# Performance work log

Measured on AMD Instinct MI355X. Metric: run time of the kernel, lower is better.

## Reference

```python
import jax, jax.numpy as jnp
import numpy as np
from jax import lax

IN_PLANES = 512
GROWTH = 32
PLANES = 4 * GROWTH  # 128
EPS = 1e-5


def setup_inputs() -> dict:
    key = jax.random.key(0)
    ks = jax.random.split(key, 10)
    x = jax.random.normal(ks[0], (128, IN_PLANES, 32, 32), dtype=jnp.float32)
    # bn1 affine params (batch-stat BN, track_running_stats=False)
    gamma1 = jax.random.normal(ks[1], (IN_PLANES,), dtype=jnp.float32) * 0.1 + 1.0
    beta1 = jax.random.normal(ks[2], (IN_PLANES,), dtype=jnp.float32) * 0.1
    # convbn1: 1x1 conv weight + folded BN (running stats)
    w1 = jax.random.normal(ks[3], (PLANES, IN_PLANES, 1, 1), dtype=jnp.float32) * (1.0 / np.sqrt(IN_PLANES))
    gamma2 = jax.random.normal(ks[4], (PLANES,), dtype=jnp.float32) * 0.1 + 1.0
    beta2 = jax.random.normal(ks[5], (PLANES,), dtype=jnp.float32) * 0.1
    mean2 = jax.random.normal(ks[6], (PLANES,), dtype=jnp.float32) * 0.1
    var2 = jax.random.uniform(ks[7], (PLANES,), dtype=jnp.float32, minval=0.5, maxval=1.5)
    # conv2: 3x3 conv, padding 1, no bias
    w2 = jax.random.normal(ks[8], (GROWTH, PLANES, 3, 3), dtype=jnp.float32) * (1.0 / np.sqrt(9 * PLANES))
    return {"x": x, "gamma1": gamma1, "beta1": beta1, "w1": w1,
            "gamma2": gamma2, "beta2": beta2, "mean2": mean2, "var2": var2,
            "w2": w2}


def _bn(h, mean, var, gamma, beta):
    # channel-wise affine normalization, NCHW
    inv = lax.rsqrt(var + EPS)
    scale = (gamma * inv)[None, :, None, None]
    shift = (beta - mean * gamma * inv)[None, :, None, None]
    return h * scale + shift


def reference(x, gamma1, beta1, w1, gamma2, beta2, mean2, var2, w2):
    # bn1: batch statistics (track_running_stats=False)
    mu = jnp.mean(x, axis=(0, 2, 3))
    var = jnp.var(x, axis=(0, 2, 3))  # biased, as torch BN normalization
    h = _bn(x, mu, var, gamma1, beta1)
    h = jax.nn.relu(h)
    # convbn1: 1x1 conv then folded BN (running stats)
    h = lax.conv_general_dilated(h, w1, (1, 1), 'VALID',
                                 dimension_numbers=('NCHW', 'OIHW', 'NCHW'))
    h = _bn(h, mean2, var2, gamma2, beta2)
    h = jax.nn.relu(h)
    # conv2: 3x3, stride 1, pad 1, no bias
    out = lax.conv_general_dilated(h, w2, (1, 1), ((1, 1), (1, 1)),
                                   dimension_numbers=('NCHW', 'OIHW', 'NCHW'))
    # dense concat along channels
    return jnp.concatenate([x, out], axis=1)
```

## Files before the change

### kernel.cpp

```cpp
#include <hip/hip_runtime.h>

#define EPS 1e-5f

typedef __bf16 bf16x8 __attribute__((ext_vector_type(8)));
typedef __bf16 bf16x4 __attribute__((ext_vector_type(4)));
typedef unsigned short ushort8 __attribute__((ext_vector_type(8)));
typedef float f32x4 __attribute__((ext_vector_type(4)));

static __device__ __forceinline__ unsigned short f2bf(float f) {
  unsigned int u = __float_as_uint(f);
  u += 0x7fffu + ((u >> 16) & 1u);
  return (unsigned short)(u >> 16);
}


__global__ void __launch_bounds__(256) k1_kernel(
    const float* __restrict__ x, float* __restrict__ out,
    float* __restrict__ psum, float* __restrict__ psq,
    const float* __restrict__ w1, const float* __restrict__ gamma2,
    const float* __restrict__ beta2, const float* __restrict__ mean2,
    const float* __restrict__ var2, const float* __restrict__ w2,
    unsigned short* __restrict__ w1b, unsigned short* __restrict__ w2b,
    float* __restrict__ bias2) {
  const int t = threadIdx.x;
  if (blockIdx.x >= 4096) {
    int idx = (blockIdx.x - 4096) * 256 + t;
    if (idx < 128 * 512) {
      int oc = idx >> 9;
      float s2 = gamma2[oc] * rsqrtf(var2[oc] + EPS);
      w1b[idx] = f2bf(w1[idx] * s2);
    } else if (idx < 128 * 512 + 32 * 1152) {
      int i2 = idx - 128 * 512;
      int oc = i2 / 1152;
      int rem = i2 - oc * 1152;
      int tap = rem >> 7;
      int c = rem & 127;
      w2b[i2] = f2bf(w2[(oc * 128 + c) * 9 + tap]);
    } else if (idx < 128 * 512 + 32 * 1152 + 128) {
      int oc = idx - (128 * 512 + 32 * 1152);
      float s2 = gamma2[oc] * rsqrtf(var2[oc] + EPS);
      bias2[oc] = beta2[oc] - mean2[oc] * s2;
    }
    return;
  }
  const int c = blockIdx.x & 511;
  const int nq = blockIdx.x >> 9;
  float sum = 0.f, sq = 0.f;
  const f32x4* __restrict__ x4 = (const f32x4*)x;
  f32x4* out4 = (f32x4*)out;
#pragma unroll 8
  for (int i = 0; i < 16; ++i) {
    const int n = nq * 16 + i;
    f32x4 v = x4[(((size_t)n * 512 + c) << 8) + t];
    __builtin_nontemporal_store(v, &out4[(((size_t)n * 544 + c) << 8) + t]);
    sum += v[0] + v[1] + v[2] + v[3];
    sq += v[0] * v[0] + v[1] * v[1] + v[2] * v[2] + v[3] * v[3];
  }
  __shared__ float ls[2][4];
  for (int off = 32; off > 0; off >>= 1) {
    sum += __shfl_down(sum, off);
    sq += __shfl_down(sq, off);
  }
  const int w = t >> 6;
  if ((t & 63) == 0) { ls[0][w] = sum; ls[1][w] = sq; }
  __syncthreads();
  if (t == 0) {
    psum[c * 8 + nq] = ls[0][0] + ls[0][1] + ls[0][2] + ls[0][3];
    psq[c * 8 + nq] = ls[1][0] + ls[1][1] + ls[1][2] + ls[1][3];
  }
}

__global__ void reduce_kernel(const float* __restrict__ psum,
                              const float* __restrict__ psq,
                              const float* __restrict__ g1,
                              const float* __restrict__ be1,
                              float* __restrict__ s1, float* __restrict__ b1) {
  int c = blockIdx.x * 256 + threadIdx.x;
  if (c < 512) {
    float S = 0.f, Q = 0.f;
#pragma unroll
    for (int q = 0; q < 8; ++q) { S += psum[c * 8 + q]; Q += psq[c * 8 + q]; }
    float mean = S * (1.0f / 131072.0f);
    float var = Q * (1.0f / 131072.0f) - mean * mean;
    float s = g1[c] * rsqrtf(var + EPS);
    s1[c] = s;
    b1[c] = be1[c] - mean * s;
  }
}

__global__ void __launch_bounds__(256, 2) conv1_kernel(
    const float* __restrict__ x, const unsigned short* __restrict__ w1b,
    const float* __restrict__ s1, const float* __restrict__ b1,
    const float* __restrict__ bias2, unsigned short* __restrict__ h2) {
  const int t = threadIdx.x;
  __shared__ float s1s[512], b1s[512];
  __shared__ __align__(16) unsigned short tile[32 * 260];
  for (int cc = t; cc < 512; cc += 256) {
    s1s[cc] = s1[cc];
    b1s[cc] = b1[cc];
  }
  __syncthreads();

  const int lane = t & 63;
  const int wv = t >> 6;
  const int n = 127 - (blockIdx.x >> 2);
  const int q = blockIdx.x & 3;
  const int l15 = lane & 15;
  const int kb = lane >> 4;

  f32x4 acc[8][4];
#pragma unroll
  for (int m = 0; m < 8; ++m)
#pragma unroll
    for (int g = 0; g < 4; ++g) acc[m][g] = (f32x4){0.f, 0.f, 0.f, 0.f};

  const f32x4* __restrict__ xq = (const f32x4*)(x + (size_t)n * 524288 + q * 256);

  f32x4 v[8];
#pragma unroll
  for (int i = 0; i < 8; ++i)
    v[i] = xq[(size_t)(wv * 8 + i) * 256 + lane];

  for (int k = 0; k < 16; ++k) {
    const int c0 = k * 32;
#pragma unroll
    for (int i = 0; i < 8; ++i) {
      const int c = c0 + wv * 8 + i;
      const float s = s1s[c], b = b1s[c];
      bf16x4 bv;
      bv[0] = (__bf16)fmaxf(fmaf(v[i][0], s, b), 0.f);
      bv[1] = (__bf16)fmaxf(fmaf(v[i][1], s, b), 0.f);
      bv[2] = (__bf16)fmaxf(fmaf(v[i][2], s, b), 0.f);
      bv[3] = (__bf16)fmaxf(fmaf(v[i][3], s, b), 0.f);
      *(bf16x4*)&tile[(size_t)(wv * 8 + i) * 260 + 4 * lane] = bv;
    }
    if (k < 15) {
#pragma unroll
      for (int i = 0; i < 8; ++i)
        v[i] = xq[(size_t)(c0 + 32 + wv * 8 + i) * 256 + lane];
    }
    __syncthreads();
    bf16x8 bf[4];
#pragma unroll
    for (int g = 0; g < 4; ++g) {
      const int pl = wv * 64 + g * 16 + l15;
      bf16x8 tmp;
#pragma unroll
      for (int j = 0; j < 8; ++j)
        tmp[j] = __builtin_bit_cast(__bf16, tile[(kb * 8 + j) * 260 + pl]);
      bf[g] = tmp;
    }
#pragma unroll
    for (int m = 0; m < 8; ++m) {
      bf16x8 af = *(const bf16x8*)(w1b + (size_t)(m * 16 + l15) * 512 + c0 + kb * 8);
#pragma unroll
      for (int g = 0; g < 4; ++g)
        acc[m][g] = __builtin_amdgcn_mfma_f32_16x16x32_bf16(af, bf[g], acc[m][g], 0, 0, 0);
    }
    __syncthreads();
  }

#pragma unroll
  for (int m = 0; m < 8; ++m) {
    const int ocb = m * 16 + kb * 4;
    float bz0 = bias2[ocb + 0], bz1 = bias2[ocb + 1];
    float bz2 = bias2[ocb + 2], bz3 = bias2[ocb + 3];
#pragma unroll
    for (int g = 0; g < 4; ++g) {
      const int p = q * 256 + wv * 64 + g * 16 + l15;
      bf16x4 hv;
      hv[0] = (__bf16)fmaxf(acc[m][g][0] + bz0, 0.f);
      hv[1] = (__bf16)fmaxf(acc[m][g][1] + bz1, 0.f);
      hv[2] = (__bf16)fmaxf(acc[m][g][2] + bz2, 0.f);
      hv[3] = (__bf16)fmaxf(acc[m][g][3] + bz3, 0.f);
      *(bf16x4*)(h2 + ((size_t)n * 1024 + p) * 128 + ocb) = hv;
    }
  }
}

__global__ void __launch_bounds__(256) conv2_kernel(
    const unsigned short* __restrict__ h2, const unsigned short* __restrict__ w2b,
    float* __restrict__ out) {
  const int t = threadIdx.x;
  const int lane = t & 63;
  const int wv = t >> 6;
  const int n = blockIdx.x >> 2;
  const int pbase = (blockIdx.x & 3) * 256 + wv * 64;
  const int l15 = lane & 15;
  const int kb = lane >> 4;

  f32x4 acc[2][4];
#pragma unroll
  for (int m = 0; m < 2; ++m)
#pragma unroll
    for (int g = 0; g < 4; ++g) acc[m][g] = (f32x4){0.f, 0.f, 0.f, 0.f};

  const unsigned short* __restrict__ h2n = h2 + (size_t)n * 1024 * 128;

#pragma unroll
  for (int tap = 0; tap < 9; ++tap) {
    const int dy = tap / 3 - 1;
    const int dx = tap % 3 - 1;
#pragma unroll
    for (int c0 = 0; c0 < 128; c0 += 32) {
      const int cb = c0 + kb * 8;
      bf16x8 af[2];
#pragma unroll
      for (int m = 0; m < 2; ++m)
        af[m] = *(const bf16x8*)(w2b + (size_t)(m * 16 + l15) * 1152 + tap * 128 + cb);
#pragma unroll
      for (int g = 0; g < 4; ++g) {
        const int p = pbase + g * 16 + l15;
        const int y = (p >> 5) & 31;
        const int xx = p & 31;
        const int y2 = y + dy;
        const int x2 = xx + dx;
        bf16x8 bv = __builtin_bit_cast(bf16x8, (ushort8){0, 0, 0, 0, 0, 0, 0, 0});
        if (y2 >= 0 && y2 < 32 && x2 >= 0 && x2 < 32)
          bv = *(const bf16x8*)(h2n + ((size_t)(y2 * 32 + x2)) * 128 + cb);
#pragma unroll
        for (int m = 0; m < 2; ++m)
          acc[m][g] = __builtin_amdgcn_mfma_f32_16x16x32_bf16(af[m], bv, acc[m][g], 0, 0, 0);
      }
    }
  }

#pragma unroll
  for (int m = 0; m < 2; ++m) {
    const int oc = m * 16 + kb * 4;
#pragma unroll
    for (int g = 0; g < 4; ++g) {
      const int p = pbase + g * 16 + l15;
#pragma unroll
      for (int r = 0; r < 4; ++r)
        __builtin_nontemporal_store(
            acc[m][g][r], &out[((size_t)n * 544 + 512 + oc + r) * 1024 + p]);
    }
  }
}

extern "C" void kernel_launch(void* const* d_in, const int* in_sizes, int n_in,
                              void* d_out, int out_size, void* d_ws, size_t ws_size,
                              hipStream_t stream) {
  const float* x = (const float*)d_in[0];
  const float* gamma1 = (const float*)d_in[1];
  const float* beta1 = (const float*)d_in[2];
  const float* w1 = (const float*)d_in[3];
  const float* gamma2 = (const float*)d_in[4];
  const float* beta2 = (const float*)d_in[5];
  const float* mean2 = (const float*)d_in[6];
  const float* var2 = (const float*)d_in[7];
  const float* w2 = (const float*)d_in[8];
  float* out = (float*)d_out;

  char* ws = (char*)d_ws;
  unsigned short* h2 = (unsigned short*)ws;
  unsigned short* w1b = (unsigned short*)(ws + 33554432);
  unsigned short* w2b = (unsigned short*)(ws + 33685504);
  float* bias2 = (float*)(ws + 33759232);
  float* s1 = (float*)(ws + 33759744);
  float* b1 = (float*)(ws + 33761792);
  float* psum = (float*)(ws + 33763840);
  float* psq = (float*)(ws + 33780224);

  k1_kernel<<<4497, 256, 0, stream>>>(x, out, psum, psq,
                                      w1, gamma2, beta2, mean2, var2, w2,
                                      w1b, w2b, bias2);
  reduce_kernel<<<2, 256, 0, stream>>>(psum, psq, gamma1, beta1, s1, b1);
  conv1_kernel<<<512, 256, 0, stream>>>(x, w1b, s1, b1, bias2, h2);
  conv2_kernel<<<512, 256, 0, stream>>>(h2, w2b, out);
}
```

Before: 199.3 us.

## Fold BN reduce into conv1, double-buffer transposed tile, halve spatial tiles

Removes the separate reduce kernel launch: each conv1 block now recomputes the per-channel BN1 scale and shift from the partial sums. The conv1 main loop uses a double-buffered, XOR-swizzled LDS tile stored position-major. This allows vectorized B-fragment reads, a single barrier per k step, and a prefetch two steps ahead. Both conv kernels switch to 128-pixel slabs with twice as many blocks, and conv1 targets 3 blocks per CU to raise occupancy. The cost is redundant per-block stat recomputation and scalar bf16 LDS stores.

Measured after the change: 268.0 us. 1.34x slower.

```diff
diff --git a/kernel.cpp b/kernel.cpp
--- a/kernel.cpp
+++ b/kernel.cpp
@@ -70,94 +70,118 @@
   }
 }
 
-__global__ void reduce_kernel(const float* __restrict__ psum,
-                              const float* __restrict__ psq,
-                              const float* __restrict__ g1,
-                              const float* __restrict__ be1,
-                              float* __restrict__ s1, float* __restrict__ b1) {
-  int c = blockIdx.x * 256 + threadIdx.x;
-  if (c < 512) {
-    float S = 0.f, Q = 0.f;
-#pragma unroll
-    for (int q = 0; q < 8; ++q) { S += psum[c * 8 + q]; Q += psq[c * 8 + q]; }
-    float mean = S * (1.0f / 131072.0f);
-    float var = Q * (1.0f / 131072.0f) - mean * mean;
-    float s = g1[c] * rsqrtf(var + EPS);
-    s1[c] = s;
-    b1[c] = be1[c] - mean * s;
-  }
-}
-
-__global__ void __launch_bounds__(256, 2) conv1_kernel(
+__global__ void __launch_bounds__(256, 3) conv1_kernel(
     const float* __restrict__ x, const unsigned short* __restrict__ w1b,
-    const float* __restrict__ s1, const float* __restrict__ b1,
+    const float* __restrict__ psum, const float* __restrict__ psq,
+    const float* __restrict__ g1, const float* __restrict__ be1,
     const float* __restrict__ bias2, unsigned short* __restrict__ h2) {
   const int t = threadIdx.x;
   __shared__ float s1s[512], b1s[512];
-  __shared__ __align__(16) unsigned short tile[32 * 260];
+  __shared__ __align__(16) unsigned short tile[2][128 * 36];
+
   for (int cc = t; cc < 512; cc += 256) {
-    s1s[cc] = s1[cc];
-    b1s[cc] = b1[cc];
+    float S = 0.f, Q = 0.f;
+#pragma unroll
+    for (int q = 0; q < 8; ++q) { S += psum[cc * 8 + q]; Q += psq[cc * 8 + q]; }
+    float mean = S * (1.0f / 131072.0f);
+    float var = Q * (1.0f / 131072.0f) - mean * mean;
+    float s = g1[cc] * rsqrtf(var + EPS);
+    s1s[cc] = s;
+    b1s[cc] = be1[cc] - mean * s;
   }
   __syncthreads();
 
   const int lane = t & 63;
   const int wv = t >> 6;
-  const int n = 127 - (blockIdx.x >> 2);
-  const int q = blockIdx.x & 3;
+  const int n = 127 - (blockIdx.x >> 3);
+  const int slab = blockIdx.x & 7;
   const int l15 = lane & 15;
   const int kb = lane >> 4;
-
-  f32x4 acc[8][4];
+  const int tg = t >> 5;
+  const int l31 = t & 31;
+  const int csw = (l31 & 3) << 3;
+
+  f32x4 acc[8][2];
 #pragma unroll
   for (int m = 0; m < 8; ++m)
 #pragma unroll
-    for (int g = 0; g < 4; ++g) acc[m][g] = (f32x4){0.f, 0.f, 0.f, 0.f};
-
-  const f32x4* __restrict__ xq = (const f32x4*)(x + (size_t)n * 524288 + q * 256);
-
-  f32x4 v[8];
-#pragma unroll
-  for (int i = 0; i < 8; ++i)
-    v[i] = xq[(size_t)(wv * 8 + i) * 256 + lane];
-
+    for (int g = 0; g < 2; ++g) acc[m][g] = (f32x4){0.f, 0.f, 0.f, 0.f};
+
+  const f32x4* __restrict__ x4 =
+      (const f32x4*)(x + (size_t)n * 524288 + slab * 128);
+
+  int rbase[2];
+#pragma unroll
+  for (int g = 0; g < 2; ++g) {
+    const int pl = wv * 32 + g * 16 + l15;
+    const int s = (pl >> 2) & 3;
+    rbase[g] = pl * 36 + ((kb ^ s) << 3);
+  }
+
+  f32x4 v[4], vn[4];
+#pragma unroll
+  for (int j2 = 0; j2 < 4; ++j2)
+    v[j2] = x4[(size_t)(j2 * 8 + tg) * 256 + l31];
+#pragma unroll
+  for (int j2 = 0; j2 < 4; ++j2) {
+    const int cl = j2 * 8 + tg;
+    const float s = s1s[cl], b = b1s[cl];
+    const int col = cl ^ csw;
+#pragma unroll
+    for (int jj = 0; jj < 4; ++jj) {
+      float a = fmaxf(fmaf(v[j2][jj], s, b), 0.f);
+      tile[0][(l31 * 4 + jj) * 36 + col] =
+          __builtin_bit_cast(unsigned short, (__bf16)a);
+    }
+  }
+#pragma unroll
+  for (int j2 = 0; j2 < 4; ++j2)
+    v[j2] = x4[(size_t)(32 + j2 * 8 + tg) * 256 + l31];
+  __syncthreads();
+
+#pragma unroll
   for (int k = 0; k < 16; ++k) {
-    const int c0 = k * 32;
-#pragma unroll
-    for (int i = 0; i < 8; ++i) {
-      const int c = c0 + wv * 8 + i;
-      const float s = s1s[c], b = b1s[c];
-      bf16x4 bv;
-      bv[0] = (__bf16)fmaxf(fmaf(v[i][0], s, b), 0.f);
-      bv[1] = (__bf16)fmaxf(fmaf(v[i][1], s, b), 0.f);
-      bv[2] = (__bf16)fmaxf(fmaf(v[i][2], s, b), 0.f);
-      bv[3] = (__bf16)fmaxf(fmaf(v[i][3], s, b), 0.f);
-      *(bf16x4*)&tile[(size_t)(wv * 8 + i) * 260 + 4 * lane] = bv;
-    }
-    if (k < 15) {
-#pragma unroll
-      for (int i = 0; i < 8; ++i)
-        v[i] = xq[(size_t)(c0 + 32 + wv * 8 + i) * 256 + lane];
+    const int buf = k & 1;
+    bf16x8 bf[2];
+#pragma unroll
+    for (int g = 0; g < 2; ++g) {
+      bf16x4 lo = *(const bf16x4*)&tile[buf][rbase[g]];
+      bf16x4 hi = *(const bf16x4*)&tile[buf][rbase[g] + 4];
+      bf16x8 bb;
+#pragma unroll
+      for (int j = 0; j < 4; ++j) { bb[j] = lo[j]; bb[j + 4] = hi[j]; }
+      bf[g] = bb;
+    }
+    if (k + 2 < 16) {
+#pragma unroll
+      for (int j2 = 0; j2 < 4; ++j2)
+        vn[j2] = x4[(size_t)((k + 2) * 32 + j2 * 8 + tg) * 256 + l31];
+    }
+#pragma unroll
+    for (int m = 0; m < 8; ++m) {
+      bf16x8 af = *(const bf16x8*)(w1b + (size_t)(m * 16 + l15) * 512 + k * 32 + kb * 8);
+#pragma unroll
+      for (int g = 0; g < 2; ++g)
+        acc[m][g] = __builtin_amdgcn_mfma_f32_16x16x32_bf16(af, bf[g], acc[m][g], 0, 0, 0);
+    }
+    if (k + 1 < 16) {
+#pragma unroll
+      for (int j2 = 0; j2 < 4; ++j2) {
+        const int cl = j2 * 8 + tg;
+        const int c = (k + 1) * 32 + cl;
+        const float s = s1s[c], b = b1s[c];
+        const int col = cl ^ csw;
+#pragma unroll
+        for (int jj = 0; jj < 4; ++jj) {
+          float a = fmaxf(fmaf(v[j2][jj], s, b), 0.f);
+          tile[buf ^ 1][(l31 * 4 + jj) * 36 + col] =
+              __builtin_bit_cast(unsigned short, (__bf16)a);
+        }
+      }
     }
     __syncthreads();
-    bf16x8 bf[4];
-#pragma unroll
-    for (int g = 0; g < 4; ++g) {
-      const int pl = wv * 64 + g * 16 + l15;
-      bf16x8 tmp;
-#pragma unroll
-      for (int j = 0; j < 8; ++j)
-        tmp[j] = __builtin_bit_cast(__bf16, tile[(kb * 8 + j) * 260 + pl]);
-      bf[g] = tmp;
-    }
-#pragma unroll
-    for (int m = 0; m < 8; ++m) {
-      bf16x8 af = *(const bf16x8*)(w1b + (size_t)(m * 16 + l15) * 512 + c0 + kb * 8);
-#pragma unroll
-      for (int g = 0; g < 4; ++g)
-        acc[m][g] = __builtin_amdgcn_mfma_f32_16x16x32_bf16(af, bf[g], acc[m][g], 0, 0, 0);
-    }
-    __syncthreads();
+#pragma unroll
+    for (int j2 = 0; j2 < 4; ++j2) v[j2] = vn[j2];
   }
 
 #pragma unroll
@@ -166,8 +190,8 @@
     float bz0 = bias2[ocb + 0], bz1 = bias2[ocb + 1];
     float bz2 = bias2[ocb + 2], bz3 = bias2[ocb + 3];
 #pragma unroll
-    for (int g = 0; g < 4; ++g) {
-      const int p = q * 256 + wv * 64 + g * 16 + l15;
+    for (int g = 0; g < 2; ++g) {
+      const int p = slab * 128 + wv * 32 + g * 16 + l15;
       bf16x4 hv;
       hv[0] = (__bf16)fmaxf(acc[m][g][0] + bz0, 0.f);
       hv[1] = (__bf16)fmaxf(acc[m][g][1] + bz1, 0.f);
@@ -184,16 +208,16 @@
   const int t = threadIdx.x;
   const int lane = t & 63;
   const int wv = t >> 6;
-  const int n = blockIdx.x >> 2;
-  const int pbase = (blockIdx.x & 3) * 256 + wv * 64;
+  const int n = blockIdx.x >> 3;
+  const int pbase = (blockIdx.x & 7) * 128 + wv * 32;
   const int l15 = lane & 15;
   const int kb = lane >> 4;
 
-  f32x4 acc[2][4];
+  f32x4 acc[2][2];
 #pragma unroll
   for (int m = 0; m < 2; ++m)
 #pragma unroll
-    for (int g = 0; g < 4; ++g) acc[m][g] = (f32x4){0.f, 0.f, 0.f, 0.f};
+    for (int g = 0; g < 2; ++g) acc[m][g] = (f32x4){0.f, 0.f, 0.f, 0.f};
 
   const unsigned short* __restrict__ h2n = h2 + (size_t)n * 1024 * 128;
 
@@ -209,7 +233,7 @@
       for (int m = 0; m < 2; ++m)
         af[m] = *(const bf16x8*)(w2b + (size_t)(m * 16 + l15) * 1152 + tap * 128 + cb);
 #pragma unroll
-      for (int g = 0; g < 4; ++g) {
+      for (int g = 0; g < 2; ++g) {
         const int p = pbase + g * 16 + l15;
         const int y = (p >> 5) & 31;
         const int xx = p & 31;
@@ -229,7 +253,7 @@
   for (int m = 0; m < 2; ++m) {
     const int oc = m * 16 + kb * 4;
 #pragma unroll
-    for (int g = 0; g < 4; ++g) {
+    for (int g = 0; g < 2; ++g) {
       const int p = pbase + g * 16 + l15;
 #pragma unroll
       for (int r = 0; r < 4; ++r)
@@ -258,15 +282,12 @@
   unsigned short* w1b = (unsigned short*)(ws + 33554432);
   unsigned short* w2b = (unsigned short*)(ws + 33685504);
   float* bias2 = (float*)(ws + 33759232);
-  float* s1 = (float*)(ws + 33759744);
-  float* b1 = (float*)(ws + 33761792);
   float* psum = (float*)(ws + 33763840);
   float* psq = (float*)(ws + 33780224);
 
   k1_kernel<<<4497, 256, 0, stream>>>(x, out, psum, psq,
                                       w1, gamma2, beta2, mean2, var2, w2,
                                       w1b, w2b, bias2);
-  reduce_kernel<<<2, 256, 0, stream>>>(psum, psq, gamma1, beta1, s1, b1);
-  conv1_kernel<<<512, 256, 0, stream>>>(x, w1b, s1, b1, bias2, h2);
-  conv2_kernel<<<512, 256, 0, stream>>>(h2, w2b, out);
-}
+  conv1_kernel<<<1024, 256, 0, stream>>>(x, w1b, psum, psq, gamma1, beta1, bias2, h2);
+  conv2_kernel<<<1024, 256, 0, stream>>>(h2, w2b, out);
+}
```
